# Performance work log

Measured on AMD Instinct MI355X. Metric: run time of the kernel, lower is better.

Reference implementation:

```python
import jax, jax.numpy as jnp
import numpy as np

NUM_FRAMES = 64
H, W = 2048, 2048
MAX_DEPTH = 12


def setup_inputs() -> dict:
    key = jax.random.key(0)
    k1, k2, k3 = jax.random.split(key, 3)
    frame_colors = jax.random.uniform(k1, (NUM_FRAMES, 3), dtype=jnp.float32)
    frame_selection = jax.random.uniform(k2, (NUM_FRAMES, 2, NUM_FRAMES), dtype=jnp.float32)
    split_ratios = jax.random.uniform(k3, (NUM_FRAMES,), dtype=jnp.float32)
    return {
        "frame_colors": frame_colors,
        "frame_selection": frame_selection,
        "split_ratios": split_ratios,
    }


def reference(frame_colors, frame_selection, split_ratios):
    """Vectorized per-pixel descent of the bounded fractal recursion.

    Instead of recursive slice-assignments with host-synced argmax/.item(),
    each pixel tracks (frame idx, region origin, region size) and descends
    MAX_DEPTH levels via gathers. Equivalent math to render_frame(0,...).
    """
    # Per-frame child indices (argmax over the selection logits).
    left_child = jnp.argmax(frame_selection[:, 0, :], axis=-1).astype(jnp.int32)   # [F]
    right_child = jnp.argmax(frame_selection[:, 1, :], axis=-1).astype(jnp.int32)  # [F]

    yy, xx = jnp.meshgrid(jnp.arange(H, dtype=jnp.int32),
                          jnp.arange(W, dtype=jnp.int32), indexing="ij")  # [H,W]

    idx = jnp.zeros((H, W), jnp.int32)   # current frame index per pixel
    y0 = jnp.zeros((H, W), jnp.int32)    # region origin
    x0 = jnp.zeros((H, W), jnp.int32)
    h = jnp.full((H, W), H, jnp.int32)   # region size
    w = jnp.full((H, W), W, jnp.int32)
    done = jnp.zeros((H, W), bool)

    for _ in range(MAX_DEPTH):
        leaf = (w < 2) | (h < 2)            # base case: region too small
        act = (~done) & (~leaf)             # pixels that descend this level
        done = done | leaf

        ratio = split_ratios[idx]                       # [H,W]
        is_vert = (idx % 2) == 1                        # split_directions = i % 2
        # left_width = max(1, int(width * ratio)); analogous top_height
        lw = jnp.maximum(1, jnp.floor(w.astype(jnp.float32) * ratio).astype(jnp.int32))
        th = jnp.maximum(1, jnp.floor(h.astype(jnp.float32) * ratio).astype(jnp.int32))

        go_left = jnp.where(is_vert, (xx - x0) < lw, (yy - y0) < th)
        child = jnp.where(go_left, left_child[idx], right_child[idx])

        nx0 = jnp.where(is_vert & (~go_left), x0 + lw, x0)
        nw = jnp.where(is_vert, jnp.where(go_left, lw, w - lw), w)
        ny0 = jnp.where((~is_vert) & (~go_left), y0 + th, y0)
        nh = jnp.where(~is_vert, jnp.where(go_left, th, h - th), h)

        idx = jnp.where(act, child, idx)
        x0 = jnp.where(act, nx0, x0)
        w = jnp.where(act, nw, w)
        y0 = jnp.where(act, ny0, y0)
        h = jnp.where(act, nh, h)

    # Fill each pixel with its leaf frame's background color -> [3, H, W]
    out = frame_colors[idx]                 # [H, W, 3]
    return jnp.transpose(out, (2, 0, 1))
```

## Files before the change

kernel.cpp:

```cpp
#include <hip/hip_runtime.h>

#define HH_DIM 2048
#define WW_DIM 2048
#define NF 64
#define MAX_DEPTH 12

__global__ void child_argmax_kernel(const float* __restrict__ sel,
                                    int* __restrict__ child) {
    int r = threadIdx.x;
    if (r < 2 * NF) {
        const float* row = sel + r * NF;
        float best = row[0];
        int bi = 0;
        #pragma unroll
        for (int j = 1; j < NF; ++j) {
            float v = row[j];
            if (v > best) { best = v; bi = j; }
        }
        child[r] = bi;
    }
}

__global__ __launch_bounds__(256)
void render_kernel(const float* __restrict__ colors,
                   const float* __restrict__ ratios,
                   const int* __restrict__ child,
                   float* __restrict__ out) {
    __shared__ float s_ratio[NF];
    __shared__ int   s_child[2 * NF];
    __shared__ float s_col[3 * NF];

    int t = threadIdx.x;
    if (t < NF)      s_ratio[t] = ratios[t];
    if (t < 2 * NF)  s_child[t] = child[t];
    if (t < 3 * NF)  s_col[t]   = colors[t];
    __syncthreads();

    int gid = blockIdx.x * 256 + t;
    int y  = gid >> 9;
    int xb = (gid & 511) << 2;

    float c0[4], c1[4], c2[4];

    #pragma unroll
    for (int p = 0; p < 4; ++p) {
        int x = xb + p;
        int idx = 0;
        int x0 = 0, y0 = 0, w = WW_DIM, h = HH_DIM;
        for (int d = 0; d < MAX_DEPTH; ++d) {
            if (w < 2 || h < 2) break;
            float ratio = s_ratio[idx];
            int ni;
            if (idx & 1) {
                int lw = (int)floorf((float)w * ratio);
                lw = lw < 1 ? 1 : lw;
                bool left = (x - x0) < lw;
                ni = left ? s_child[2 * idx] : s_child[2 * idx + 1];
                if (left) { w = lw; }
                else      { x0 += lw; w -= lw; }
            } else {
                int th = (int)floorf((float)h * ratio);
                th = th < 1 ? 1 : th;
                bool left = (y - y0) < th;
                ni = left ? s_child[2 * idx] : s_child[2 * idx + 1];
                if (left) { h = th; }
                else      { y0 += th; h -= th; }
            }
            idx = ni;
        }
        c0[p] = s_col[idx * 3 + 0];
        c1[p] = s_col[idx * 3 + 1];
        c2[p] = s_col[idx * 3 + 2];
    }

    int base = y * WW_DIM + xb;
    const int plane = HH_DIM * WW_DIM;
    *(float4*)(out + base)             = make_float4(c0[0], c0[1], c0[2], c0[3]);
    *(float4*)(out + plane + base)     = make_float4(c1[0], c1[1], c1[2], c1[3]);
    *(float4*)(out + 2 * plane + base) = make_float4(c2[0], c2[1], c2[2], c2[3]);
}

extern "C" void kernel_launch(void* const* d_in, const int* in_sizes, int n_in,
                              void* d_out, int out_size, void* d_ws, size_t ws_size,
                              hipStream_t stream) {
    const float* frame_colors    = (const float*)d_in[0];
    const float* frame_selection = (const float*)d_in[1];
    const float* split_ratios    = (const float*)d_in[2];
    float* out = (float*)d_out;
    int* child = (int*)d_ws;

    child_argmax_kernel<<<1, 128, 0, stream>>>(frame_selection, child);

    render_kernel<<<4096, 256, 0, stream>>>(frame_colors, split_ratios, child, out);
}
```

Measured before the change: 98.10 us.

## Descend once per 4-pixel group, splitting only when a vertical cut divides it

Each thread now runs the tree descent once for its whole 4-pixel group and falls back to per-pixel descent only when a vertical split boundary lands inside the group. The prep kernel packs the ratio and both child indices into one float2 per node, and colors into float4, so each level needs one shared-memory load. The aim is to cut the redundant per-pixel ALU and LDS work. The divergent fallback path adds code complexity and warp divergence near boundaries.

```diff
diff --git a/kernel.cpp b/kernel.cpp
--- a/kernel.cpp
+++ b/kernel.cpp
@@ -5,11 +5,15 @@
 #define NF 64
 #define MAX_DEPTH 12
 
-__global__ void child_argmax_kernel(const float* __restrict__ sel,
-                                    int* __restrict__ child) {
-    int r = threadIdx.x;
-    if (r < 2 * NF) {
-        const float* row = sel + r * NF;
+__global__ void prep_kernel(const float* __restrict__ sel,
+                            const float* __restrict__ ratios,
+                            const float* __restrict__ colors,
+                            float2* __restrict__ node,
+                            float4* __restrict__ cpack) {
+    __shared__ int s_child[2 * NF];
+    int t = threadIdx.x;
+    if (t < 2 * NF) {
+        const float* row = sel + t * NF;
         float best = row[0];
         int bi = 0;
         #pragma unroll
@@ -17,67 +21,96 @@
             float v = row[j];
             if (v > best) { best = v; bi = j; }
         }
-        child[r] = bi;
+        s_child[t] = bi;
+    }
+    __syncthreads();
+    if (t < NF) {
+        int packed = s_child[2 * t] | (s_child[2 * t + 1] << 16);
+        node[t] = make_float2(ratios[t], __int_as_float(packed));
+        cpack[t] = make_float4(colors[3 * t], colors[3 * t + 1], colors[3 * t + 2], 0.0f);
     }
 }
 
 __global__ __launch_bounds__(256)
-void render_kernel(const float* __restrict__ colors,
-                   const float* __restrict__ ratios,
-                   const int* __restrict__ child,
+void render_kernel(const float2* __restrict__ node,
+                   const float4* __restrict__ cpack,
                    float* __restrict__ out) {
-    __shared__ float s_ratio[NF];
-    __shared__ int   s_child[2 * NF];
-    __shared__ float s_col[3 * NF];
+    __shared__ float2 s_node[NF];
+    __shared__ float4 s_col[NF];
 
     int t = threadIdx.x;
-    if (t < NF)      s_ratio[t] = ratios[t];
-    if (t < 2 * NF)  s_child[t] = child[t];
-    if (t < 3 * NF)  s_col[t]   = colors[t];
+    if (t < NF)            s_node[t] = node[t];
+    else if (t < 2 * NF)   s_col[t - NF] = cpack[t - NF];
     __syncthreads();
 
     int gid = blockIdx.x * 256 + t;
     int y  = gid >> 9;
     int xb = (gid & 511) << 2;
 
-    float c0[4], c1[4], c2[4];
+    int idx = 0, rx = xb, ry = y, w = WW_DIM, h = HH_DIM;
+    int d = 0;
+    bool div = false;
+    for (; d < MAX_DEPTH; ++d) {
+        if (w < 2 || h < 2) break;
+        float2 nd = s_node[idx];
+        int pk = __float_as_int(nd.y);
+        int lc = pk & 0xffff, rcld = pk >> 16;
+        bool vert = (idx & 1) != 0;
+        int cs  = vert ? w  : h;
+        int rc0 = vert ? rx : ry;
+        int ls = (int)((float)cs * nd.x);
+        ls = ls < 1 ? 1 : ls;
+        if (vert & (rx < ls) & (ls <= rx + 3)) { div = true; break; }
+        bool left = rc0 < ls;
+        idx = left ? lc : rcld;
+        int nr = left ? rc0 : rc0 - ls;
+        int ns = left ? ls  : cs - ls;
+        if (vert) { rx = nr; w = ns; } else { ry = nr; h = ns; }
+    }
 
-    #pragma unroll
-    for (int p = 0; p < 4; ++p) {
-        int x = xb + p;
-        int idx = 0;
-        int x0 = 0, y0 = 0, w = WW_DIM, h = HH_DIM;
-        for (int d = 0; d < MAX_DEPTH; ++d) {
-            if (w < 2 || h < 2) break;
-            float ratio = s_ratio[idx];
-            int ni;
-            if (idx & 1) {
-                int lw = (int)floorf((float)w * ratio);
-                lw = lw < 1 ? 1 : lw;
-                bool left = (x - x0) < lw;
-                ni = left ? s_child[2 * idx] : s_child[2 * idx + 1];
-                if (left) { w = lw; }
-                else      { x0 += lw; w -= lw; }
-            } else {
-                int th = (int)floorf((float)h * ratio);
-                th = th < 1 ? 1 : th;
-                bool left = (y - y0) < th;
-                ni = left ? s_child[2 * idx] : s_child[2 * idx + 1];
-                if (left) { h = th; }
-                else      { y0 += th; h -= th; }
+    int fidx0 = idx, fidx1 = idx, fidx2 = idx, fidx3 = idx;
+
+    if (div) {
+        int pidx[4], prx[4], pry[4], pw[4], ph[4];
+        #pragma unroll
+        for (int p = 0; p < 4; ++p) {
+            pidx[p] = idx; prx[p] = rx + p; pry[p] = ry; pw[p] = w; ph[p] = h;
+        }
+        #pragma unroll 1
+        for (int dd = d; dd < MAX_DEPTH; ++dd) {
+            #pragma unroll
+            for (int p = 0; p < 4; ++p) {
+                float2 nd = s_node[pidx[p]];
+                int pk = __float_as_int(nd.y);
+                int lc = pk & 0xffff, rcld = pk >> 16;
+                bool vert = (pidx[p] & 1) != 0;
+                int cs  = vert ? pw[p]  : ph[p];
+                int rc0 = vert ? prx[p] : pry[p];
+                int ls = (int)((float)cs * nd.x);
+                ls = ls < 1 ? 1 : ls;
+                bool left = rc0 < ls;
+                bool act = (pw[p] > 1) && (ph[p] > 1);
+                int child = left ? lc : rcld;
+                pidx[p] = act ? child : pidx[p];
+                int nr = left ? rc0 : rc0 - ls;
+                int ns = left ? ls  : cs - ls;
+                if (vert) { prx[p] = nr; pw[p] = ns; }
+                else      { pry[p] = nr; ph[p] = ns; }
             }
-            idx = ni;
         }
-        c0[p] = s_col[idx * 3 + 0];
-        c1[p] = s_col[idx * 3 + 1];
-        c2[p] = s_col[idx * 3 + 2];
+        fidx0 = pidx[0]; fidx1 = pidx[1]; fidx2 = pidx[2]; fidx3 = pidx[3];
     }
+
+    float4 k0 = s_col[fidx0];
+    float4 k1 = s_col[fidx1];
+    float4 k2 = s_col[fidx2];
+    float4 k3 = s_col[fidx3];
 
     int base = y * WW_DIM + xb;
     const int plane = HH_DIM * WW_DIM;
-    *(float4*)(out + base)             = make_float4(c0[0], c0[1], c0[2], c0[3]);
-    *(float4*)(out + plane + base)     = make_float4(c1[0], c1[1], c1[2], c1[3]);
-    *(float4*)(out + 2 * plane + base) = make_float4(c2[0], c2[1], c2[2], c2[3]);
+    *(float4*)(out + base)             = make_float4(k0.x, k1.x, k2.x, k3.x);
+    *(float4*)(out + plane + base)     = make_float4(k0.y, k1.y, k2.y, k3.y);
+    *(float4*)(out + 2 * plane + base) = make_float4(k0.z, k1.z, k2.z, k3.z);
 }
 
 extern "C" void kernel_launch(void* const* d_in, const int* in_sizes, int n_in,
@@ -87,9 +120,11 @@
     const float* frame_selection = (const float*)d_in[1];
     const float* split_ratios    = (const float*)d_in[2];
     float* out = (float*)d_out;
-    int* child = (int*)d_ws;
 
-    child_argmax_kernel<<<1, 128, 0, stream>>>(frame_selection, child);
+    float2* node  = (float2*)d_ws;
+    float4* cpack = (float4*)((char*)d_ws + 1024);
 
-    render_kernel<<<4096, 256, 0, stream>>>(frame_colors, split_ratios, child, out);
+    prep_kernel<<<1, 128, 0, stream>>>(frame_selection, split_ratios,
+                                       frame_colors, node, cpack);
+    render_kernel<<<4096, 256, 0, stream>>>(node, cpack, out);
 }
```

Measured after the change: 99.85 us. About the same (+1.8%).

## Build leaf rectangles in one block, then fill them as spans

Applied to the files above, without the earlier changes.

Replaces the per-pixel 12-level tree descent with a single-block breadth-first expansion of the split tree. It emits leaf rectangles, chunked to at most about 1024 pixels each, into a workspace list. A second kernel then fills each rectangle with its frame colour using scalar stores across the three planes. This removes the per-pixel descent arithmetic, but serialises tree construction in one workgroup, drops the float4 vectorised stores, and caps the item list at a fixed size.

```diff
diff --git a/kernel.cpp b/kernel.cpp
--- a/kernel.cpp
+++ b/kernel.cpp
@@ -4,80 +4,171 @@
 #define WW_DIM 2048
 #define NF 64
 #define MAX_DEPTH 12
+#define MAX_ITEMS 32768
 
-__global__ void child_argmax_kernel(const float* __restrict__ sel,
-                                    int* __restrict__ child) {
-    int r = threadIdx.x;
-    if (r < 2 * NF) {
-        const float* row = sel + r * NF;
-        float best = row[0];
-        int bi = 0;
-        #pragma unroll
-        for (int j = 1; j < NF; ++j) {
-            float v = row[j];
-            if (v > best) { best = v; bi = j; }
-        }
-        child[r] = bi;
+__device__ __forceinline__ uint2 enc(int x0, int y0, int idx, int w, int h) {
+    return make_uint2((unsigned)x0 | ((unsigned)y0 << 11) | ((unsigned)idx << 22),
+                      (unsigned)w | ((unsigned)h << 12));
+}
+
+__device__ __forceinline__ unsigned wave_iscan(unsigned x, int lane) {
+    #pragma unroll
+    for (int off = 1; off < 64; off <<= 1) {
+        unsigned v = __shfl_up(x, off);
+        if (lane >= off) x += v;
     }
+    return x;
+}
+
+__device__ __forceinline__ int calc_nit(int w, int h) {
+    int rpc = 1024 / w; if (rpc < 1) rpc = 1;
+    return (h + rpc - 1) / rpc;
+}
+
+__device__ __forceinline__ int emit_rect(uint2* __restrict__ items, int s,
+                                         int x0, int y0, int w, int h, int idx) {
+    int rpc = 1024 / w; if (rpc < 1) rpc = 1;
+    int nit = (h + rpc - 1) / rpc;
+    for (int k = 0; k < nit; ++k) {
+        int r0 = k * rpc;
+        int hc = h - r0; if (hc > rpc) hc = rpc;
+        if (s < MAX_ITEMS) items[s] = enc(x0, y0 + r0, idx, w, hc);
+        ++s;
+    }
+    return s;
 }
 
 __global__ __launch_bounds__(256)
-void render_kernel(const float* __restrict__ colors,
-                   const float* __restrict__ ratios,
-                   const int* __restrict__ child,
-                   float* __restrict__ out) {
+void build_kernel(const float* __restrict__ sel,
+                  const float* __restrict__ ratios,
+                  const float* __restrict__ colors,
+                  float4* __restrict__ cpack,
+                  int* __restrict__ item_count,
+                  uint2* __restrict__ items) {
     __shared__ float s_ratio[NF];
     __shared__ int   s_child[2 * NF];
-    __shared__ float s_col[3 * NF];
+    __shared__ uint2 s_nodes[2][2048];
+    __shared__ int   s_cnt[2];
+    __shared__ int   s_items;
 
     int t = threadIdx.x;
-    if (t < NF)      s_ratio[t] = ratios[t];
-    if (t < 2 * NF)  s_child[t] = child[t];
-    if (t < 3 * NF)  s_col[t]   = colors[t];
+    int lane = t & 63, wid = t >> 6;
+
+    if (t < 2 * NF) {
+        const float* row = sel + t * NF;
+        float best = row[0]; int bi = 0;
+        #pragma unroll
+        for (int j = 1; j < NF; ++j) { float v = row[j]; if (v > best) { best = v; bi = j; } }
+        s_child[t] = bi;
+    }
+    if (t < NF) {
+        s_ratio[t] = ratios[t];
+        cpack[t] = make_float4(colors[3*t], colors[3*t+1], colors[3*t+2], 0.0f);
+    }
+    if (t == 0) {
+        s_cnt[0] = 1; s_cnt[1] = 0; s_items = 0;
+        s_nodes[0][0] = enc(0, 0, 0, WW_DIM, HH_DIM);
+    }
     __syncthreads();
 
-    int gid = blockIdx.x * 256 + t;
-    int y  = gid >> 9;
-    int xb = (gid & 511) << 2;
+    for (int d = 0; d < MAX_DEPTH; ++d) {
+        int cur = d & 1, nx = cur ^ 1;
+        int n = s_cnt[cur];
+        bool last = (d == MAX_DEPTH - 1);
+        for (int base = wid * 64; base < n; base += 256) {
+            int i = base + lane;
+            bool valid = i < n;
+            int x0 = 0, y0 = 0, idx = 0, w = 1, h = 1;
+            bool split = false;
+            if (valid) {
+                uint2 nd = s_nodes[cur][i];
+                x0 = nd.x & 0x7FF; y0 = (nd.x >> 11) & 0x7FF; idx = (int)(nd.x >> 22);
+                w = nd.y & 0xFFF;  h = (nd.y >> 12) & 0xFFF;
+                split = (w >= 2) && (h >= 2);
+            }
+            int lw = 1, lx0 = x0, ly0 = y0, lwid = w, lhgt = h,
+                rx0 = x0, ry0 = y0, rwid = w, rhgt = h, lc = 0, rc = 0;
+            if (valid && split) {
+                float ratio = s_ratio[idx];
+                lc = s_child[2 * idx]; rc = s_child[2 * idx + 1];
+                if (idx & 1) {
+                    lw = (int)floorf((float)w * ratio); if (lw < 1) lw = 1;
+                    lwid = lw;          rhgt = h;
+                    rx0 = x0 + lw;      rwid = w - lw;
+                } else {
+                    lw = (int)floorf((float)h * ratio); if (lw < 1) lw = 1;
+                    lhgt = lw;
+                    ry0 = y0 + lw;      rhgt = h - lw;
+                }
+            }
+            unsigned nchild = 0, nit = 0;
+            if (valid) {
+                if (split && !last) nchild = 2;
+                else if (split && last)
+                    nit = (unsigned)(calc_nit(lwid, lhgt) + calc_nit(rwid, rhgt));
+                else
+                    nit = (unsigned)calc_nit(w, h);
+            }
+            unsigned incC = wave_iscan(nchild, lane);
+            unsigned incI = wave_iscan(nit, lane);
+            unsigned totC = __shfl(incC, 63);
+            unsigned totI = __shfl(incI, 63);
+            int bC = 0, bI = 0;
+            if (lane == 63) {
+                if (totC) bC = atomicAdd(&s_cnt[nx], (int)totC);
+                if (totI) bI = atomicAdd(&s_items, (int)totI);
+            }
+            bC = __shfl(bC, 63);
+            bI = __shfl(bI, 63);
+            int cslot = bC + (int)(incC - nchild);
+            int islot = bI + (int)(incI - nit);
 
-    float c0[4], c1[4], c2[4];
+            if (valid && nchild) {
+                s_nodes[nx][cslot]     = enc(lx0, ly0, lc, lwid, lhgt);
+                s_nodes[nx][cslot + 1] = enc(rx0, ry0, rc, rwid, rhgt);
+            }
+            if (valid && nit) {
+                int s = islot;
+                if (split) {
+                    s = emit_rect(items, s, lx0, ly0, lwid, lhgt, lc);
+                    s = emit_rect(items, s, rx0, ry0, rwid, rhgt, rc);
+                } else {
+                    s = emit_rect(items, s, x0, y0, w, h, idx);
+                }
+            }
+        }
+        __syncthreads();
+        if (t == 0) s_cnt[cur] = 0;
+        __syncthreads();
+    }
+    if (t == 0) *item_count = (s_items < MAX_ITEMS) ? s_items : MAX_ITEMS;
+}
 
-    #pragma unroll
-    for (int p = 0; p < 4; ++p) {
-        int x = xb + p;
-        int idx = 0;
-        int x0 = 0, y0 = 0, w = WW_DIM, h = HH_DIM;
-        for (int d = 0; d < MAX_DEPTH; ++d) {
-            if (w < 2 || h < 2) break;
-            float ratio = s_ratio[idx];
-            int ni;
-            if (idx & 1) {
-                int lw = (int)floorf((float)w * ratio);
-                lw = lw < 1 ? 1 : lw;
-                bool left = (x - x0) < lw;
-                ni = left ? s_child[2 * idx] : s_child[2 * idx + 1];
-                if (left) { w = lw; }
-                else      { x0 += lw; w -= lw; }
-            } else {
-                int th = (int)floorf((float)h * ratio);
-                th = th < 1 ? 1 : th;
-                bool left = (y - y0) < th;
-                ni = left ? s_child[2 * idx] : s_child[2 * idx + 1];
-                if (left) { h = th; }
-                else      { y0 += th; h -= th; }
-            }
-            idx = ni;
+__global__ __launch_bounds__(256)
+void fill_kernel(const float4* __restrict__ cpack,
+                 const int* __restrict__ item_count,
+                 const uint2* __restrict__ items,
+                 float* __restrict__ out) {
+    const int plane = HH_DIM * WW_DIM;
+    int count = *item_count;
+    for (int it = blockIdx.x; it < count; it += gridDim.x) {
+        uint2 v = items[it];
+        int x0 = v.x & 0x7FF, y0 = (v.x >> 11) & 0x7FF, idx = (int)(v.x >> 22);
+        int w = v.y & 0xFFF,  hc = (int)((v.y >> 12) & 0xFFF);
+        float4 col = cpack[idx];
+        int n = w * hc;
+        float rw = 1.0f / (float)w;
+        for (int p = threadIdx.x; p < n; p += 256) {
+            int r = (int)((float)p * rw);
+            int c = p - r * w;
+            if (c < 0)       { r -= 1; c += w; }
+            else if (c >= w) { r += 1; c -= w; }
+            int off = (y0 + r) * WW_DIM + x0 + c;
+            out[off]             = col.x;
+            out[plane + off]     = col.y;
+            out[2 * plane + off] = col.z;
         }
-        c0[p] = s_col[idx * 3 + 0];
-        c1[p] = s_col[idx * 3 + 1];
-        c2[p] = s_col[idx * 3 + 2];
     }
-
-    int base = y * WW_DIM + xb;
-    const int plane = HH_DIM * WW_DIM;
-    *(float4*)(out + base)             = make_float4(c0[0], c0[1], c0[2], c0[3]);
-    *(float4*)(out + plane + base)     = make_float4(c1[0], c1[1], c1[2], c1[3]);
-    *(float4*)(out + 2 * plane + base) = make_float4(c2[0], c2[1], c2[2], c2[3]);
 }
 
 extern "C" void kernel_launch(void* const* d_in, const int* in_sizes, int n_in,
@@ -87,9 +178,12 @@
     const float* frame_selection = (const float*)d_in[1];
     const float* split_ratios    = (const float*)d_in[2];
     float* out = (float*)d_out;
-    int* child = (int*)d_ws;
 
-    child_argmax_kernel<<<1, 128, 0, stream>>>(frame_selection, child);
+    float4* cpack   = (float4*)d_ws;
+    int*    count   = (int*)((char*)d_ws + 1024);
+    uint2*  items   = (uint2*)((char*)d_ws + 1088);
 
-    render_kernel<<<4096, 256, 0, stream>>>(frame_colors, split_ratios, child, out);
+    build_kernel<<<1, 256, 0, stream>>>(frame_selection, split_ratios,
+                                        frame_colors, cpack, count, items);
+    fill_kernel<<<4096, 256, 0, stream>>>(cpack, count, items, out);
 }
```

Result: slower. 141.7 us (+44.5%).
